# Kernel optimization log

Hardware: AMD Instinct MI355X
Metric: run time of the kernel (lower is better)

## Reference

```python
import math
import jax, jax.numpy as jnp
import numpy as np

D_MODEL = 1024
CONTEXT = 4
MAX_LEN = 1024
FUDGE = 0.01
MIN_PERIOD = 1.0
MAX_PERIOD = 1024.0
FORGOTTEN_AT = 0.01
F32_MAX = 3.4028235e38
LIMIT = math.log(F32_MAX) / MAX_LEN - FUDGE  # ~0.0766


def setup_inputs() -> dict:
    key = jax.random.key(0)
    k1, k2, k3 = jax.random.split(key, 3)
    B, T = 8, 512
    x = jax.random.normal(k1, (B, T, D_MODEL, 1), dtype=jnp.float32)
    memory_real = jax.random.normal(k2, (B, 1, D_MODEL, CONTEXT), dtype=jnp.float32)
    memory_imag = jax.random.normal(k3, (B, 1, D_MODEL, CONTEXT), dtype=jnp.float32)
    # 'linspace' init from __init__
    a_low = -LIMIT + FUDGE
    soft_high = math.log(FORGOTTEN_AT) / MAX_PERIOD  # modify_real=True
    a_high = max(min(-1e-06, soft_high), a_low)
    a = jnp.linspace(a_low, a_high, D_MODEL, dtype=jnp.float32)          # [F]
    b = (2.0 * jnp.pi / jnp.linspace(MIN_PERIOD, MAX_PERIOD, CONTEXT)).astype(jnp.float32)  # [C]
    return {"x": x, "memory_real": memory_real, "memory_imag": memory_imag, "a": a, "b": b}


def _psi(t, a, b):
    """t: [T] float32 -> [1, T, F, C] complex64 kernel exp((a + i b) * t)."""
    ac = jnp.clip(a, -LIMIT, -1e-08)                       # clamp as in psi()
    ab = ac[:, None] + 1j * b[None, :]                      # [F, C] complex
    return jnp.exp(ab[None, None, :, :] * t[None, :, None, None].astype(jnp.complex64))


def _batched_update(x, memory, a, b):
    # x: [B,T,F,1] real; memory: [B,1,F,C] complex
    T = x.shape[1]
    tf = jnp.float32
    inner = jnp.arange(MAX_LEN - 1, MAX_LEN - 1 - T, -1, dtype=tf)   # inner_idx[:T]
    outer = -inner                                                    # outer_idx[:T]
    offset = jnp.arange(1, T + 1, dtype=tf)                           # state_offset[:T]
    z = jnp.cumsum(_psi(inner, a, b) * x, axis=1)                     # [B,T,F,C] complex
    out = _psi(outer, a, b) * z + memory * _psi(offset, a, b)
    return out.astype(jnp.complex64)


def _forward(x, memory, a, b):
    T = x.shape[1]
    if T == 1:
        return x + memory * _psi(jnp.ones((1,), jnp.float32), a, b)
    elif T < MAX_LEN:
        return _batched_update(x, memory, a, b)
    else:
        states = []
        for s in range(0, T, MAX_LEN):
            chunk = x[:, s:s + MAX_LEN]
            memory = _batched_update(chunk, memory[:, -1:], a, b)
            states.append(memory)
        return jnp.concatenate(states, axis=1)


def reference(x, memory_real, memory_imag, a, b):
    memory = (memory_real + 1j * memory_imag).astype(jnp.complex64)  # [B,1,F,C]
    return _forward(x, memory, a, b)  # [B,T,F,C] complex64
```

## Files before the change

### kernel.cpp

```cpp
#include <hip/hip_runtime.h>
#include <math.h>


#define BB 8
#define TT 512
#define FF 1024
#define CC 4
#define NCH 16
#define LL (TT / NCH)
#define LIMIT_F 0.07664339751178941f

__device__ __forceinline__ void make_lambda(const float* __restrict__ a_vec,
                                            const float* __restrict__ b_vec,
                                            int f, float lr[CC], float li[CC])
{
    const float af = fminf(fmaxf(a_vec[f], -LIMIT_F), -1e-8f);
    const float ea = expf(af);
#pragma unroll
    for (int c = 0; c < CC; ++c) {
        float s, cz;
        sincosf(b_vec[c], &s, &cz);
        lr[c] = ea * cz;
        li[c] = ea * s;
    }
}

__global__ __launch_bounds__(256) void
p1_kernel(const float* __restrict__ x,
          const float* __restrict__ a_vec,
          const float* __restrict__ b_vec,
          float* __restrict__ ws_e,
          long long x_lim, long long ws_lim)
{
    const int g = blockIdx.x * 256 + threadIdx.x;
    const int f = g & (FF - 1);
    const int b = (g >> 10) & (BB - 1);
    const int j = g >> 13;

    float lr[CC], li[CC];
    make_lambda(a_vec, b_vec, f, lr, li);

    const long long xbase = ((long long)b * TT + j * LL) * FF + f;
    const bool xok = (xbase + (long long)(LL - 1) * FF) < x_lim;

    float sr[CC] = {0.f, 0.f, 0.f, 0.f}, si[CC] = {0.f, 0.f, 0.f, 0.f};
#pragma unroll 4
    for (int t = 0; t < LL; ++t) {
        const float xv = xok ? x[xbase + (long long)t * FF] : 0.f;
#pragma unroll
        for (int c = 0; c < CC; ++c) {
            const float nr = fmaf(lr[c], sr[c], fmaf(-li[c], si[c], xv));
            const float ni = fmaf(li[c], sr[c], lr[c] * si[c]);
            sr[c] = nr; si[c] = ni;
        }
    }
    const long long w = (((long long)j * BB + b) * FF + f) * 8;
    if (w + 7 < ws_lim) {
        float4* w4 = (float4*)(ws_e + w);
        w4[0] = make_float4(sr[0], si[0], sr[1], si[1]);
        w4[1] = make_float4(sr[2], si[2], sr[3], si[3]);
    }
}

__global__ __launch_bounds__(256) void
comb_kernel(const float* __restrict__ mem_r,
            const float* __restrict__ mem_i,
            const float* __restrict__ a_vec,
            const float* __restrict__ b_vec,
            const float* __restrict__ ws_e,
            float* __restrict__ ws_s,
            long long mem_lim, long long ws_lim)
{
    const int g = blockIdx.x * 256 + threadIdx.x;
    const int c = g & 3;
    const int f = (g >> 2) & (FF - 1);
    const int b = g >> 12;

    const float af = fminf(fmaxf(a_vec[f], -LIMIT_F), -1e-8f);
    const float eaL = expf(af * (float)LL);
    float sL, cL;
    sincosf(b_vec[c] * (float)LL, &sL, &cL);
    const float lLr = eaL * cL, lLi = eaL * sL;

    const long long m = (long long)(b * FF + f) * CC + c;
    float Sr = (m < mem_lim) ? mem_r[m] : 0.f;
    float Si = (m < mem_lim) ? mem_i[m] : 0.f;

    const long long base = ((long long)b * FF + f) * 8 + 2 * c;
    const long long slab = (long long)BB * FF * 8;
    for (int j = 0; j < NCH; ++j) {
        const long long o = (long long)j * slab + base;
        if (o + 1 < ws_lim) { ws_s[o] = Sr; ws_s[o + 1] = Si; }
        float er = 0.f, ei = 0.f;
        if (o + 1 < ws_lim) { er = ws_e[o]; ei = ws_e[o + 1]; }
        const float nr = fmaf(lLr, Sr, fmaf(-lLi, Si, er));
        const float ni = fmaf(lLi, Sr, fmaf(lLr, Si, ei));
        Sr = nr; Si = ni;
    }
}

__global__ __launch_bounds__(256) void
p2_kernel(const float* __restrict__ x,
          const float* __restrict__ a_vec,
          const float* __restrict__ b_vec,
          const float* __restrict__ ws_s,
          float* __restrict__ out,
          long long x_lim, long long ws_lim, long long out4_lim,
          long long imag_off4)
{
    const int g = blockIdx.x * 256 + threadIdx.x;
    const int f = g & (FF - 1);
    const int b = (g >> 10) & (BB - 1);
    const int j = g >> 13;

    float lr[CC], li[CC];
    make_lambda(a_vec, b_vec, f, lr, li);

    float sr[CC] = {0.f, 0.f, 0.f, 0.f}, si[CC] = {0.f, 0.f, 0.f, 0.f};
    const long long sidx = (((long long)j * BB + b) * FF + f) * 8;
    if (sidx + 7 < ws_lim) {
        const float4* s4 = (const float4*)(ws_s + sidx);
        const float4 A = s4[0], Bv = s4[1];
        sr[0] = A.x;  si[0] = A.y;  sr[1] = A.z;  si[1] = A.w;
        sr[2] = Bv.x; si[2] = Bv.y; sr[3] = Bv.z; si[3] = Bv.w;
    }

    const long long xbase = ((long long)b * TT + j * LL) * FF + f;
    const bool xok = (xbase + (long long)(LL - 1) * FF) < x_lim;

    float4* out4 = (float4*)out;
    const long long obase = xbase;
    const bool rok = (obase + (long long)(LL - 1) * FF) < out4_lim;
    const bool iok = (imag_off4 > 0) &&
                     ((obase + imag_off4 + (long long)(LL - 1) * FF) < out4_lim);

#pragma unroll 4
    for (int t = 0; t < LL; ++t) {
        const float xv = xok ? x[xbase + (long long)t * FF] : 0.f;
#pragma unroll
        for (int c = 0; c < CC; ++c) {
            const float nr = fmaf(lr[c], sr[c], fmaf(-li[c], si[c], xv));
            const float ni = fmaf(li[c], sr[c], lr[c] * si[c]);
            sr[c] = nr; si[c] = ni;
        }
        if (rok) out4[obase + (long long)t * FF] =
            make_float4(sr[0], sr[1], sr[2], sr[3]);
        if (iok) out4[obase + imag_off4 + (long long)t * FF] =
            make_float4(si[0], si[1], si[2], si[3]);
    }
}

__global__ __launch_bounds__(256) void
fb_kernel(const float* __restrict__ x,
          const float* __restrict__ mem_r,
          const float* __restrict__ mem_i,
          const float* __restrict__ a_vec,
          const float* __restrict__ b_vec,
          float* __restrict__ out,
          long long x_lim, long long mem_lim, long long out4_lim,
          long long imag_off4)
{
    const int g = blockIdx.x * 256 + threadIdx.x;
    const int f = g & (FF - 1);
    const int b = g >> 10;

    float lr[CC], li[CC];
    make_lambda(a_vec, b_vec, f, lr, li);

    float sr[CC], si[CC];
#pragma unroll
    for (int c = 0; c < CC; ++c) {
        const long long m = (long long)(b * FF + f) * CC + c;
        sr[c] = (m < mem_lim) ? mem_r[m] : 0.f;
        si[c] = (m < mem_lim) ? mem_i[m] : 0.f;
    }

    const long long xbase = (long long)b * TT * FF + f;
    const bool xok = (xbase + (long long)(TT - 1) * FF) < x_lim;
    float4* out4 = (float4*)out;
    const bool rok = (xbase + (long long)(TT - 1) * FF) < out4_lim;
    const bool iok = (imag_off4 > 0) &&
                     ((xbase + imag_off4 + (long long)(TT - 1) * FF) < out4_lim);

    for (int t = 0; t < TT; ++t) {
        const float xv = xok ? x[xbase + (long long)t * FF] : 0.f;
#pragma unroll
        for (int c = 0; c < CC; ++c) {
            const float nr = fmaf(lr[c], sr[c], fmaf(-li[c], si[c], xv));
            const float ni = fmaf(li[c], sr[c], lr[c] * si[c]);
            sr[c] = nr; si[c] = ni;
        }
        if (rok) out4[xbase + (long long)t * FF] =
            make_float4(sr[0], sr[1], sr[2], sr[3]);
        if (iok) out4[xbase + imag_off4 + (long long)t * FF] =
            make_float4(si[0], si[1], si[2], si[3]);
    }
}

extern "C" void kernel_launch(void* const* d_in, const int* in_sizes, int n_in,
                              void* d_out, int out_size, void* d_ws, size_t ws_size,
                              hipStream_t stream)
{
    const float* x     = (const float*)d_in[0];
    const float* mem_r = (const float*)d_in[1];
    const float* mem_i = (const float*)d_in[2];
    const float* a_vec = (const float*)d_in[3];
    const float* b_vec = (const float*)d_in[4];
    float* out = (float*)d_out;

    const long long x_lim   = (long long)in_sizes[0];
    const long long mem_lim = (long long)in_sizes[1];
    const long long BTFC = (long long)BB * TT * FF * CC;
    const long long out4_lim = (long long)out_size / 4;
    const long long imag_off4 = ((long long)out_size >= 2 * BTFC) ? (BTFC / 4) : 0;

    const long long buf_floats = (long long)NCH * BB * FF * 8;
    if (ws_size >= (size_t)(2 * buf_floats) * sizeof(float)) {
        float* ws_e = (float*)d_ws;
        float* ws_s = ws_e + buf_floats;
        p1_kernel<<<(BB * FF * NCH) / 256, 256, 0, stream>>>(
            x, a_vec, b_vec, ws_e, x_lim, buf_floats);
        comb_kernel<<<(BB * FF * CC) / 256, 256, 0, stream>>>(
            mem_r, mem_i, a_vec, b_vec, ws_e, ws_s, mem_lim, buf_floats);
        p2_kernel<<<(BB * FF * NCH) / 256, 256, 0, stream>>>(
            x, a_vec, b_vec, ws_s, out, x_lim, buf_floats, out4_lim, imag_off4);
    } else {
        fb_kernel<<<(BB * FF) / 256, 256, 0, stream>>>(
            x, mem_r, mem_i, a_vec, b_vec, out,
            x_lim, mem_lim, out4_lim, imag_off4);
    }
}
```

Before: 108.0 us.

## Fuse chunk-carry combine into second pass and double chunk count

Removes the separate combine kernel: each second-pass thread now rebuilds its chunk's starting state by scanning all earlier chunk end-states from the workspace, using a precomputed lambda^L. The chunk count goes from 16 to 32, which doubles parallelism and halves each chunk's serial length. The chunk loops are fully unrolled and the output stores become nontemporal. In exchange there is redundant O(j) prefix work per thread, more workspace reads for later chunks, and a different combine order that can change floating-point rounding.

```diff
diff --git a/kernel.cpp b/kernel.cpp
--- a/kernel.cpp
+++ b/kernel.cpp
@@ -6,9 +6,11 @@
 #define TT 512
 #define FF 1024
 #define CC 4
-#define NCH 16
+#define NCH 32
 #define LL (TT / NCH)
 #define LIMIT_F 0.07664339751178941f
+
+typedef float v4f __attribute__((ext_vector_type(4)));
 
 __device__ __forceinline__ void make_lambda(const float* __restrict__ a_vec,
                                             const float* __restrict__ b_vec,
@@ -24,6 +26,8 @@
         li[c] = ea * s;
     }
 }
+
+#define WSE(j, b, f) ((((long long)(j) * BB + (b)) * FF + (f)) * 8)
 
 __global__ __launch_bounds__(256) void
 p1_kernel(const float* __restrict__ x,
@@ -44,7 +48,7 @@
     const bool xok = (xbase + (long long)(LL - 1) * FF) < x_lim;
 
     float sr[CC] = {0.f, 0.f, 0.f, 0.f}, si[CC] = {0.f, 0.f, 0.f, 0.f};
-#pragma unroll 4
+#pragma unroll
     for (int t = 0; t < LL; ++t) {
         const float xv = xok ? x[xbase + (long long)t * FF] : 0.f;
 #pragma unroll
@@ -54,59 +58,24 @@
             sr[c] = nr; si[c] = ni;
         }
     }
-    const long long w = (((long long)j * BB + b) * FF + f) * 8;
+    const long long w = WSE(j, b, f);
     if (w + 7 < ws_lim) {
-        float4* w4 = (float4*)(ws_e + w);
-        w4[0] = make_float4(sr[0], si[0], sr[1], si[1]);
-        w4[1] = make_float4(sr[2], si[2], sr[3], si[3]);
-    }
-}
-
-__global__ __launch_bounds__(256) void
-comb_kernel(const float* __restrict__ mem_r,
-            const float* __restrict__ mem_i,
-            const float* __restrict__ a_vec,
-            const float* __restrict__ b_vec,
-            const float* __restrict__ ws_e,
-            float* __restrict__ ws_s,
-            long long mem_lim, long long ws_lim)
-{
-    const int g = blockIdx.x * 256 + threadIdx.x;
-    const int c = g & 3;
-    const int f = (g >> 2) & (FF - 1);
-    const int b = g >> 12;
-
-    const float af = fminf(fmaxf(a_vec[f], -LIMIT_F), -1e-8f);
-    const float eaL = expf(af * (float)LL);
-    float sL, cL;
-    sincosf(b_vec[c] * (float)LL, &sL, &cL);
-    const float lLr = eaL * cL, lLi = eaL * sL;
-
-    const long long m = (long long)(b * FF + f) * CC + c;
-    float Sr = (m < mem_lim) ? mem_r[m] : 0.f;
-    float Si = (m < mem_lim) ? mem_i[m] : 0.f;
-
-    const long long base = ((long long)b * FF + f) * 8 + 2 * c;
-    const long long slab = (long long)BB * FF * 8;
-    for (int j = 0; j < NCH; ++j) {
-        const long long o = (long long)j * slab + base;
-        if (o + 1 < ws_lim) { ws_s[o] = Sr; ws_s[o + 1] = Si; }
-        float er = 0.f, ei = 0.f;
-        if (o + 1 < ws_lim) { er = ws_e[o]; ei = ws_e[o + 1]; }
-        const float nr = fmaf(lLr, Sr, fmaf(-lLi, Si, er));
-        const float ni = fmaf(lLi, Sr, fmaf(lLr, Si, ei));
-        Sr = nr; Si = ni;
+        v4f* w4 = (v4f*)(ws_e + w);
+        w4[0] = (v4f){sr[0], si[0], sr[1], si[1]};
+        w4[1] = (v4f){sr[2], si[2], sr[3], si[3]};
     }
 }
 
 __global__ __launch_bounds__(256) void
 p2_kernel(const float* __restrict__ x,
+          const float* __restrict__ mem_r,
+          const float* __restrict__ mem_i,
           const float* __restrict__ a_vec,
           const float* __restrict__ b_vec,
-          const float* __restrict__ ws_s,
+          const float* __restrict__ ws_e,
           float* __restrict__ out,
-          long long x_lim, long long ws_lim, long long out4_lim,
-          long long imag_off4)
+          long long x_lim, long long mem_lim, long long ws_lim,
+          long long out4_lim, long long imag_off4)
 {
     const int g = blockIdx.x * 256 + threadIdx.x;
     const int f = g & (FF - 1);
@@ -116,25 +85,51 @@
     float lr[CC], li[CC];
     make_lambda(a_vec, b_vec, f, lr, li);
 
-    float sr[CC] = {0.f, 0.f, 0.f, 0.f}, si[CC] = {0.f, 0.f, 0.f, 0.f};
-    const long long sidx = (((long long)j * BB + b) * FF + f) * 8;
-    if (sidx + 7 < ws_lim) {
-        const float4* s4 = (const float4*)(ws_s + sidx);
-        const float4 A = s4[0], Bv = s4[1];
-        sr[0] = A.x;  si[0] = A.y;  sr[1] = A.z;  si[1] = A.w;
-        sr[2] = Bv.x; si[2] = Bv.y; sr[3] = Bv.z; si[3] = Bv.w;
+    const float af = fminf(fmaxf(a_vec[f], -LIMIT_F), -1e-8f);
+    const float eaL = expf(af * (float)LL);
+    float lLr[CC], lLi[CC];
+#pragma unroll
+    for (int c = 0; c < CC; ++c) {
+        float s, cz;
+        sincosf(b_vec[c] * (float)LL, &s, &cz);
+        lLr[c] = eaL * cz;
+        lLi[c] = eaL * s;
+    }
+
+    float sr[CC], si[CC];
+#pragma unroll
+    for (int c = 0; c < CC; ++c) {
+        const long long m = (long long)(b * FF + f) * CC + c;
+        sr[c] = (m < mem_lim) ? mem_r[m] : 0.f;
+        si[c] = (m < mem_lim) ? mem_i[m] : 0.f;
+    }
+
+    for (int i = 0; i < j; ++i) {
+        const long long w = WSE(i, b, f);
+        v4f A = (v4f){0.f, 0.f, 0.f, 0.f}, Bv = A;
+        if (w + 7 < ws_lim) {
+            const v4f* w4 = (const v4f*)(ws_e + w);
+            A = w4[0]; Bv = w4[1];
+        }
+        const float er[CC] = {A.x, A.z, Bv.x, Bv.z};
+        const float ei[CC] = {A.y, A.w, Bv.y, Bv.w};
+#pragma unroll
+        for (int c = 0; c < CC; ++c) {
+            const float nr = fmaf(lLr[c], sr[c], fmaf(-lLi[c], si[c], er[c]));
+            const float ni = fmaf(lLi[c], sr[c], fmaf(lLr[c], si[c], ei[c]));
+            sr[c] = nr; si[c] = ni;
+        }
     }
 
     const long long xbase = ((long long)b * TT + j * LL) * FF + f;
     const bool xok = (xbase + (long long)(LL - 1) * FF) < x_lim;
-
-    float4* out4 = (float4*)out;
+    v4f* out4 = (v4f*)out;
     const long long obase = xbase;
     const bool rok = (obase + (long long)(LL - 1) * FF) < out4_lim;
     const bool iok = (imag_off4 > 0) &&
                      ((obase + imag_off4 + (long long)(LL - 1) * FF) < out4_lim);
 
-#pragma unroll 4
+#pragma unroll
     for (int t = 0; t < LL; ++t) {
         const float xv = xok ? x[xbase + (long long)t * FF] : 0.f;
 #pragma unroll
@@ -143,10 +138,12 @@
             const float ni = fmaf(li[c], sr[c], lr[c] * si[c]);
             sr[c] = nr; si[c] = ni;
         }
-        if (rok) out4[obase + (long long)t * FF] =
-            make_float4(sr[0], sr[1], sr[2], sr[3]);
-        if (iok) out4[obase + imag_off4 + (long long)t * FF] =
-            make_float4(si[0], si[1], si[2], si[3]);
+        if (rok) __builtin_nontemporal_store(
+            (v4f){sr[0], sr[1], sr[2], sr[3]},
+            &out4[obase + (long long)t * FF]);
+        if (iok) __builtin_nontemporal_store(
+            (v4f){si[0], si[1], si[2], si[3]},
+            &out4[obase + imag_off4 + (long long)t * FF]);
     }
 }
 
@@ -177,7 +174,7 @@
 
     const long long xbase = (long long)b * TT * FF + f;
     const bool xok = (xbase + (long long)(TT - 1) * FF) < x_lim;
-    float4* out4 = (float4*)out;
+    v4f* out4 = (v4f*)out;
     const bool rok = (xbase + (long long)(TT - 1) * FF) < out4_lim;
     const bool iok = (imag_off4 > 0) &&
                      ((xbase + imag_off4 + (long long)(TT - 1) * FF) < out4_lim);
@@ -191,9 +188,9 @@
             sr[c] = nr; si[c] = ni;
         }
         if (rok) out4[xbase + (long long)t * FF] =
-            make_float4(sr[0], sr[1], sr[2], sr[3]);
+            (v4f){sr[0], sr[1], sr[2], sr[3]};
         if (iok) out4[xbase + imag_off4 + (long long)t * FF] =
-            make_float4(si[0], si[1], si[2], si[3]);
+            (v4f){si[0], si[1], si[2], si[3]};
     }
 }
 
@@ -214,16 +211,15 @@
     const long long out4_lim = (long long)out_size / 4;
     const long long imag_off4 = ((long long)out_size >= 2 * BTFC) ? (BTFC / 4) : 0;
 
-    const long long buf_floats = (long long)NCH * BB * FF * 8;
-    if (ws_size >= (size_t)(2 * buf_floats) * sizeof(float)) {
+    const long long ws_floats = (long long)NCH * BB * FF * 8;
+    if (ws_size >= (size_t)ws_floats * sizeof(float)) {
         float* ws_e = (float*)d_ws;
-        float* ws_s = ws_e + buf_floats;
-        p1_kernel<<<(BB * FF * NCH) / 256, 256, 0, stream>>>(
-            x, a_vec, b_vec, ws_e, x_lim, buf_floats);
-        comb_kernel<<<(BB * FF * CC) / 256, 256, 0, stream>>>(
-            mem_r, mem_i, a_vec, b_vec, ws_e, ws_s, mem_lim, buf_floats);
-        p2_kernel<<<(BB * FF * NCH) / 256, 256, 0, stream>>>(
-            x, a_vec, b_vec, ws_s, out, x_lim, buf_floats, out4_lim, imag_off4);
+        const int threads = BB * FF * NCH;
+        p1_kernel<<<threads / 256, 256, 0, stream>>>(
+            x, a_vec, b_vec, ws_e, x_lim, ws_floats);
+        p2_kernel<<<threads / 256, 256, 0, stream>>>(
+            x, mem_r, mem_i, a_vec, b_vec, ws_e, out,
+            x_lim, mem_lim, ws_floats, out4_lim, imag_off4);
     } else {
         fb_kernel<<<(BB * FF) / 256, 256, 0, stream>>>(
             x, mem_r, mem_i, a_vec, b_vec, out,
```

Result: faster. 104.7 us (-3.0%).
